# Performance work log

Hardware: AMD Instinct MI355X
Metric: run time of the kernel (lower is better)

## Reference

```python
import jax, jax.numpy as jnp
import numpy as np

B, S, HID, H, DH = 4, 1024, 1024, 16, 64
MAX_REL = 16
SCALE = 1.0 / (DH ** 0.5)


def _rel_bias(emb, seq_len):
    # Shaw-style relative position bias: emb is [2*MAX_REL+1, DH]
    pos = jnp.arange(seq_len)
    dist = jnp.clip(pos[None, :] - pos[:, None], -MAX_REL, MAX_REL) + MAX_REL
    return emb[dist]  # [S, S, DH]


def setup_inputs() -> dict:
    key = jax.random.key(0)
    ks = jax.random.split(key, 14)
    n = jax.random.normal
    w = 0.02
    return {
        "query": n(ks[0], (B, S, HID), dtype=jnp.float32),
        "key": n(ks[1], (B, S, HID), dtype=jnp.float32),
        "value": n(ks[2], (B, S, HID), dtype=jnp.float32),
        # per-head projection weights stacked over heads
        "Wq": n(ks[3], (H, HID, DH), dtype=jnp.float32) * w,
        "bq": n(ks[4], (H, DH), dtype=jnp.float32) * w,
        "Wk": n(ks[5], (H, HID, DH), dtype=jnp.float32) * w,
        "bk": n(ks[6], (H, DH), dtype=jnp.float32) * w,
        "Wv": n(ks[7], (H, HID, DH), dtype=jnp.float32) * w,
        "bv": n(ks[8], (H, DH), dtype=jnp.float32) * w,
        # relative-position embedding tables (shared across heads)
        "rel_k_emb": n(ks[9], (2 * MAX_REL + 1, DH), dtype=jnp.float32) * w,
        "rel_v_emb": n(ks[10], (2 * MAX_REL + 1, DH), dtype=jnp.float32) * w,
        # output projection fc: Linear(hidden, hidden)
        "fc_W": n(ks[11], (HID, HID), dtype=jnp.float32) * w,
        "fc_b": n(ks[12], (HID,), dtype=jnp.float32) * w,
    }


def reference(query, key, value, Wq, bq, Wk, bk, Wv, bv, rel_k_emb, rel_v_emb, fc_W, fc_b):
    # per-head projections, all heads batched: [B, H, S, DH]
    q = jnp.einsum('bsd,hde->bhse', query, Wq) + bq[None, :, None, :]
    k = jnp.einsum('bsd,hde->bhse', key, Wk) + bk[None, :, None, :]
    v = jnp.einsum('bsd,hde->bhse', value, Wv) + bv[None, :, None, :]

    k_bias = _rel_bias(rel_k_emb, S)  # [S, S, DH]
    v_bias = _rel_bias(rel_v_emb, S)  # [S, S, DH]

    # scores: QK^T plus relative-position key bias term
    scores = jnp.einsum('bhqe,bhke->bhqk', q, k)
    scores = scores + jnp.einsum('bhqe,qke->bhqk', q, k_bias)
    attn = jax.nn.softmax(scores * SCALE, axis=-1)  # [B, H, S, S]

    # values: A V plus relative-position value bias term
    out = jnp.einsum('bhqk,bhke->bhqe', attn, v)
    out = out + jnp.einsum('bhqk,qke->bhqe', attn, v_bias)

    # concat heads -> [B, S, HID], then fc
    out = out.transpose(0, 2, 1, 3).reshape(B, S, HID)
    return out @ fc_W.T + fc_b
```

## Files before the change

### kernel.cpp

```cpp
#include <hip/hip_runtime.h>
#include <stdint.h>

#define B_ 4
#define S_ 1024
#define HID_ 1024
#define H_ 16
#define DH_ 64
#define NDIST 33
#define SCALE_ 0.125f

typedef unsigned short u16;
typedef __attribute__((ext_vector_type(8))) short short8;
typedef __attribute__((ext_vector_type(4))) float floatx4;

static __device__ __forceinline__ float bf2f(u16 u) {
  union { unsigned int i; float f; } v; v.i = ((unsigned int)u) << 16; return v.f;
}
static __device__ __forceinline__ u16 f2bf(float x) {
  union { float f; unsigned int i; } v; v.f = x;
  return (u16)((v.i + 0x7FFFu + ((v.i >> 16) & 1u)) >> 16);
}
static __device__ __forceinline__ floatx4 mfma_bf16(short8 a, short8 b, floatx4 c) {
  return __builtin_amdgcn_mfma_f32_16x16x32_bf16(a, b, c, 0, 0, 0);
}
static __device__ __forceinline__ void gload_lds16(const void* g, void* l) {
  __builtin_amdgcn_global_load_lds(
      (const __attribute__((address_space(1))) unsigned int*)g,
      (__attribute__((address_space(3))) unsigned int*)l, 16, 0, 0);
}

#define OFF_BQ   0
#define OFF_BK   1024
#define OFF_BV   2048
#define OFF_RELK 3072
#define OFF_RELV 5184
#define OFF_FCW  7296
#define OFF_FCB  1055872
#define CONV_TOT 1056896

struct SrcPtrs { const void* p[7]; };

__global__ __launch_bounds__(256) void detect_kernel(const u16* __restrict__ q,
                                                     int* __restrict__ flag) {
  __shared__ float red[256];
  float m = 0.f;
  for (int i = threadIdx.x; i < 8192; i += 256) {
    float v = fabsf(bf2f(q[2 * i]));
    m = fmaxf(m, (v < 1e30f) ? v : 1e20f);
  }
  red[threadIdx.x] = m;
  __syncthreads();
  for (int s = 128; s > 0; s >>= 1) {
    if (threadIdx.x < (unsigned)s) red[threadIdx.x] = fmaxf(red[threadIdx.x], red[threadIdx.x + s]);
    __syncthreads();
  }
  if (threadIdx.x == 0) *flag = (red[0] > 1e4f) ? 1 : 0;
}

__global__ __launch_bounds__(256) void convert_kernel(SrcPtrs srcs,
                                                      const int* __restrict__ flag,
                                                      u16* __restrict__ dst) {
  constexpr int segsz[7] = {1024,1024,1024,2112,2112,1048576,1024};
  constexpr int cumE[7]  = {OFF_BQ,OFF_BK,OFF_BV,OFF_RELK,OFF_RELV,OFF_FCW,OFF_FCB};
  constexpr int cumB[8]  = {0,1,2,3,6,9,1033,1034};
  const int bid = blockIdx.x;
  int t = 0;
  #pragma unroll
  for (int i = 1; i < 7; ++i) if (bid >= cumB[i]) t = i;
  const int chunk = (bid - cumB[t]) * 1024 + threadIdx.x * 4;
  if (chunk >= segsz[t]) return;
  __align__(8) u16 o[4];
  if (*flag) {
    const float* s = (const float*)srcs.p[t];
    float4 v = *(const float4*)(s + chunk);
    o[0] = f2bf(v.x); o[1] = f2bf(v.y); o[2] = f2bf(v.z); o[3] = f2bf(v.w);
  } else {
    const u16* s = (const u16*)srcs.p[t];
    *(uint2*)o = *(const uint2*)(s + chunk);
  }
  *(uint2*)(dst + cumE[t] + chunk) = *(const uint2*)o;
}

__global__ __launch_bounds__(256) void qkvconv_kernel(
    const void* __restrict__ qin, const void* __restrict__ kin,
    const void* __restrict__ vin, const int* __restrict__ flag,
    u16* __restrict__ qc, u16* __restrict__ kc, u16* __restrict__ vc)
{
  const int isf = *flag;
  const int total = 3 * (4096 * 1024 / 8);
  for (int g = blockIdx.x * 256 + threadIdx.x; g < total; g += gridDim.x * 256) {
    const int z = g >> 19;
    const int off = (g & 524287) * 8;
    const void* src = (z == 0) ? qin : (z == 1) ? kin : vin;
    u16* dst = (z == 0) ? qc : (z == 1) ? kc : vc;
    if (isf) {
      const float* s = (const float*)src + off;
      float4 v0 = *(const float4*)s;
      float4 v1 = *(const float4*)(s + 4);
      __align__(16) u16 tmp[8] = {f2bf(v0.x),f2bf(v0.y),f2bf(v0.z),f2bf(v0.w),
                                  f2bf(v1.x),f2bf(v1.y),f2bf(v1.z),f2bf(v1.w)};
      *(uint4*)(dst + off) = *(const uint4*)tmp;
    } else {
      *(uint4*)(dst + off) = *(const uint4*)((const u16*)src + off);
    }
  }
}

__global__ __launch_bounds__(256) void wtrans_kernel(
    const void* __restrict__ Wq, const void* __restrict__ Wk, const void* __restrict__ Wv,
    const int* __restrict__ flag, u16* __restrict__ wt)
{
  const int dt = blockIdx.x, h = blockIdx.y, z = blockIdx.z;
  const void* W = (z == 0) ? Wq : (z == 1) ? Wk : Wv;
  const int tid = threadIdx.x;
  const int isf = *flag;
  __shared__ __align__(16) u16 t_l[64 * 72];

  #pragma unroll
  for (int i = 0; i < 2; ++i) {
    int g = tid + 256 * i;
    int d = g & 63, e8 = (g >> 6) * 8;
    size_t off = ((size_t)h * HID_ + dt * 64 + d) * DH_ + e8;
    __align__(16) u16 tmp[8];
    if (isf) {
      const float* Wf = (const float*)W + off;
      float4 v0 = *(const float4*)Wf;
      float4 v1 = *(const float4*)(Wf + 4);
      tmp[0]=f2bf(v0.x); tmp[1]=f2bf(v0.y); tmp[2]=f2bf(v0.z); tmp[3]=f2bf(v0.w);
      tmp[4]=f2bf(v1.x); tmp[5]=f2bf(v1.y); tmp[6]=f2bf(v1.z); tmp[7]=f2bf(v1.w);
    } else {
      *(uint4*)tmp = *(const uint4*)((const u16*)W + off);
    }
    #pragma unroll
    for (int j = 0; j < 8; ++j) {
      int e = e8 + j;
      t_l[e * 72 + (((d >> 3) ^ (e & 7)) << 3) + (d & 7)] = tmp[j];
    }
  }
  __syncthreads();
  {
    int e = tid >> 2, c0 = (tid & 3) * 2;
    u16* dst = wt + ((size_t)(z * H_ + h) * DH_ + e) * HID_ + dt * 64;
    uint4 x0 = *(const uint4*)(t_l + e * 72 + (((c0    ) ^ (e & 7)) << 3));
    uint4 x1 = *(const uint4*)(t_l + e * 72 + (((c0 + 1) ^ (e & 7)) << 3));
    *(uint4*)(dst + c0 * 8)     = x0;
    *(uint4*)(dst + c0 * 8 + 8) = x1;
  }
}

__global__ __launch_bounds__(256, 3) void proj_kernel(
    const u16* __restrict__ qc, const u16* __restrict__ kc, const u16* __restrict__ vc,
    const u16* __restrict__ wt, const u16* __restrict__ conv,
    u16* __restrict__ qo, u16* __restrict__ ko, u16* __restrict__ vo)
{
  const int bid = blockIdx.x + 32 * (blockIdx.y + 8 * blockIdx.z);
  const int xcd = bid & 7, local = bid >> 3;
  const int p  = xcd * 3 + (local >> 5);
  const int rt = local & 31;
  const int z  = p >> 3, ct = p & 7;

  const u16* A    = (z == 0) ? qc : (z == 1) ? kc : vc;
  const u16* Wz   = wt + (size_t)z * (H_ * DH_ * HID_);
  const u16* bias = conv + ((z == 0) ? OFF_BQ : (z == 1) ? OFF_BK : OFF_BV);
  u16*       O    = (z == 0) ? qo : (z == 1) ? ko : vo;
  const int tid = threadIdx.x, lane = tid & 63, w = tid >> 6, quad = lane >> 4, l16 = lane & 15;

  __shared__ __align__(16) u16 a_l[2][128 * 32];
  __shared__ __align__(16) u16 b_l[2][128 * 32];

  floatx4 acc[4][4];
  #pragma unroll
  for (int i = 0; i < 4; ++i)
    #pragma unroll
    for (int j = 0; j < 4; ++j) acc[i][j] = (floatx4){0.f,0.f,0.f,0.f};

  const int mq = (w & 1) * 64, nq = (w >> 1) * 64;
  const int u = (lane & 3) ^ ((lane >> 3) & 3);
  const int cs = (quad ^ ((l16 >> 1) & 3)) * 8;

  auto STAGE = [&](int bu, int kk) {
    #pragma unroll
    for (int i = 0; i < 2; ++i) {
      int row = (tid + 256 * i) >> 2;
      gload_lds16(A  + (size_t)(rt * 128 + row) * HID_ + kk * 32 + u * 8,
                  a_l[bu] + (w * 64 + i * 256) * 8);
      gload_lds16(Wz + (size_t)(ct * 128 + row) * HID_ + kk * 32 + u * 8,
                  b_l[bu] + (w * 64 + i * 256) * 8);
    }
  };

  STAGE(0, 0);
  int cur = 0;
  for (int kk = 0; kk < 32; ++kk) {
    __syncthreads();
    if (kk + 1 < 32) STAGE(cur ^ 1, kk + 1);
    const u16* ab = a_l[cur];
    const u16* bb = b_l[cur];
    short8 af[4], bfr[4];
    #pragma unroll
    for (int i = 0; i < 4; ++i) {
      af[i]  = *(const short8*)(ab + (mq + i * 16 + l16) * 32 + cs);
      bfr[i] = *(const short8*)(bb + (nq + i * 16 + l16) * 32 + cs);
    }
    #pragma unroll
    for (int i = 0; i < 4; ++i)
      #pragma unroll
      for (int j = 0; j < 4; ++j)
        acc[i][j] = mfma_bf16(af[i], bfr[j], acc[i][j]);
    cur ^= 1;
  }

  #pragma unroll
  for (int j = 0; j < 4; ++j) {
    int col = ct * 128 + nq + j * 16 + l16;
    int hh = col >> 6, e = col & 63;
    float bb = bf2f(bias[hh * 64 + e]);
    #pragma unroll
    for (int i = 0; i < 4; ++i) {
      #pragma unroll
      for (int r = 0; r < 4; ++r) {
        int m = rt * 128 + mq + i * 16 + quad * 4 + r;
        int bidx = m >> 10, srow = m & 1023;
        O[(((size_t)(bidx * H_ + hh)) * S_ + srow) * DH_ + e] = f2bf(acc[i][j][r] + bb);
      }
    }
  }
}

__global__ __launch_bounds__(256, 4) void attn_kernel(
    const u16* __restrict__ Q, const u16* __restrict__ K, const u16* __restrict__ V,
    const u16* __restrict__ conv, u16* __restrict__ Ox)
{
  const int bid = blockIdx.x + 16 * (blockIdx.y + 16 * blockIdx.z);
  const int nid = (bid & 7) * 128 + (bid >> 3);
  const int qt = nid & 15, h = (nid >> 4) & 15, b = nid >> 8;

  const int tid = threadIdx.x;
  const int lane = tid & 63, w = tid >> 6, quad = lane >> 4, l16 = lane & 15;
  const size_t base = ((size_t)(b * H_ + h)) * S_ * DH_;
  const u16* Kb = K + base;
  const u16* Vb = V + base;

  __shared__ __align__(16) char smem[40320];
  u16*   p_l    = (u16*)(smem);
  u16*   q_l    = p_l;
  u16*   k_l    = (u16*)(smem + 9216);
  u16*   vt_l   = (u16*)(smem + 18432);
  u16*   rq_l   = (u16*)(smem + 27648);
  float* bucket = (float*)(smem + 31872);
  u16*   rkb    = (u16*)(smem + 31872);

  uint4 kr0 = *(const uint4*)(Kb + (size_t)(tid >> 3) * DH_ + (tid & 7) * 8);
  uint4 kr1 = *(const uint4*)(Kb + (size_t)((tid >> 3) + 32) * DH_ + (tid & 7) * 8);
  uint4 vr0 = *(const uint4*)(Vb + (size_t)lane * DH_ + w * 16);
  uint4 vr1 = *(const uint4*)(Vb + (size_t)lane * DH_ + w * 16 + 8);

  #pragma unroll
  for (int i = 0; i < 2; ++i) {
    int idx = tid + 256 * i;
    int row = idx >> 3, c8 = (idx & 7) * 8;
    *(uint4*)(q_l + row * 72 + c8) =
        *(const uint4*)(Q + base + (size_t)(qt * 64 + row) * DH_ + c8);
  }
  const u16* relk = conv + OFF_RELK;
  for (int idx = tid; idx < 48 * 8; idx += 256) {
    int row = idx >> 3, c8 = (idx & 7) * 8;
    uint4 v = make_uint4(0, 0, 0, 0);
    if (row < NDIST) v = *(const uint4*)(relk + row * 64 + c8);
    *(uint4*)(rkb + row * 72 + c8) = v;
  }
  __syncthreads();

  const int m0 = w * 16;
  short8 qa0 = *(const short8*)(q_l + (m0 + l16) * 72 + quad * 8);
  short8 qa1 = *(const short8*)(q_l + (m0 + l16) * 72 + 32 + quad * 8);

  floatx4 c_d0 = {0.f,0.f,0.f,0.f}, c_d32 = {0.f,0.f,0.f,0.f};
  #pragma unroll
  for (int t3 = 0; t3 < 3; ++t3) {
    floatx4 c = {0.f,0.f,0.f,0.f};
    c = mfma_bf16(qa0, *(const short8*)(rkb + (t3 * 16 + l16) * 72 + quad * 8), c);
    c = mfma_bf16(qa1, *(const short8*)(rkb + (t3 * 16 + l16) * 72 + 32 + quad * 8), c);
    if (t3 == 0) c_d0 = c;
    if (t3 == 2) c_d32 = c;
    int d = t3 * 16 + l16;
    if (d < NDIST) {
      #pragma unroll
      for (int r = 0; r < 4; ++r) rq_l[(m0 + quad * 4 + r) * 33 + d] = f2bf(c[r]);
    }
  }
  float rqs_lo[4], rqs_hi[4];
  #pragma unroll
  for (int r = 0; r < 4; ++r) {
    rqs_lo[r] = bf2f(f2bf(__shfl(c_d0[r],  lane & 48, 64))) * SCALE_;
    rqs_hi[r] = bf2f(f2bf(__shfl(c_d32[r], lane & 48, 64))) * SCALE_;
  }
  __syncthreads();
  for (int idx = tid; idx < 64 * 33; idx += 256) bucket[idx] = 0.f;

  floatx4 o[4], oi = {0.f,0.f,0.f,0.f};
  #pragma unroll
  for (int t = 0; t < 4; ++t) o[t] = (floatx4){0.f,0.f,0.f,0.f};

  for (int kt = 0; kt < 16; ++kt) {
    __syncthreads();
    *(uint4*)(k_l + (tid >> 3) * 72 + (tid & 7) * 8) = kr0;
    *(uint4*)(k_l + ((tid >> 3) + 32) * 72 + (tid & 7) * 8) = kr1;
    {
      const u16* t8 = (const u16*)&vr0;
      #pragma unroll
      for (int j = 0; j < 8; ++j) vt_l[(w * 16 + j) * 72 + lane] = t8[j];
      const u16* t9 = (const u16*)&vr1;
      #pragma unroll
      for (int j = 0; j < 8; ++j) vt_l[(w * 16 + 8 + j) * 72 + lane] = t9[j];
    }
    __syncthreads();
    if (kt < 15) {
      const size_t kb = (size_t)((kt + 1) * 64);
      kr0 = *(const uint4*)(Kb + (kb + (tid >> 3)) * DH_ + (tid & 7) * 8);
      kr1 = *(const uint4*)(Kb + (kb + (tid >> 3) + 32) * DH_ + (tid & 7) * 8);
      vr0 = *(const uint4*)(Vb + (kb + lane) * DH_ + w * 16);
      vr1 = *(const uint4*)(Vb + (kb + lane) * DH_ + w * 16 + 8);
    }

    const int dkt = kt - qt;
    const bool near = (dkt >= -1) && (dkt <= 1);

    #pragma unroll
    for (int t = 0; t < 4; ++t) {
      floatx4 s = {0.f,0.f,0.f,0.f};
      s = mfma_bf16(qa0, *(const short8*)(k_l + (t * 16 + l16) * 72 + quad * 8), s);
      s = mfma_bf16(qa1, *(const short8*)(k_l + (t * 16 + l16) * 72 + 32 + quad * 8), s);
      int kcol = t * 16 + l16;
      if (near) {
        #pragma unroll
        for (int r = 0; r < 4; ++r) {
          int m = m0 + quad * 4 + r;
          int delta = (kt * 64 + kcol) - (qt * 64 + m);
          int dist = (delta < -16 ? -16 : (delta > 16 ? 16 : delta)) + 16;
          float logit = (s[r] + bf2f(rq_l[m * 33 + dist])) * SCALE_;
          u16 pu = f2bf(__expf(fminf(logit, 30.f)));
          p_l[m * 72 + kcol] = pu;
          float pv = bf2f(pu);
          float vhi = (dist == 32) ? pv : 0.f;
          float vlo = (dist == 0) ? pv : 0.f;
          #pragma unroll
          for (int off2 = 1; off2 < 16; off2 <<= 1) {
            vhi += __shfl_xor(vhi, off2, 16);
            vlo += __shfl_xor(vlo, off2, 16);
          }
          if (l16 == 0) {
            if (vhi != 0.f) atomicAdd(&bucket[m * 33 + 32], vhi);
            if (vlo != 0.f) atomicAdd(&bucket[m * 33 + 0], vlo);
          }
          if (dist > 0 && dist < 32) atomicAdd(&bucket[m * 33 + dist], pv);
        }
      } else {
        #pragma unroll
        for (int r = 0; r < 4; ++r) {
          int m = m0 + quad * 4 + r;
          float logit = fmaf(s[r], SCALE_, (dkt < 0) ? rqs_lo[r] : rqs_hi[r]);
          u16 pu = f2bf(__expf(fminf(logit, 30.f)));
          p_l[m * 72 + kcol] = pu;
        }
      }
    }

    u16 iv = ((l16 == 0 && dkt <= -2) || (l16 == 1 && dkt >= 2)) ? (u16)0x3F80 : (u16)0;
    short8 ib;
    #pragma unroll
    for (int j = 0; j < 8; ++j) ib[j] = (short)iv;
    short8 pa0 = *(const short8*)(p_l + (m0 + l16) * 72 + quad * 8);
    short8 pa1 = *(const short8*)(p_l + (m0 + l16) * 72 + 32 + quad * 8);
    oi = mfma_bf16(pa0, ib, oi);
    oi = mfma_bf16(pa1, ib, oi);
    #pragma unroll
    for (int t = 0; t < 4; ++t) {
      int e = t * 16 + l16;
      short8 vb0 = *(const short8*)(vt_l + e * 72 + quad * 8);
      short8 vb1 = *(const short8*)(vt_l + e * 72 + 32 + quad * 8);
      o[t] = mfma_bf16(pa0, vb0, o[t]);
      o[t] = mfma_bf16(pa1, vb1, o[t]);
    }
  }

  __syncthreads();
  if (l16 == 0) {
    #pragma unroll
    for (int r = 0; r < 4; ++r) bucket[(m0 + quad * 4 + r) * 33 + 0] += oi[r];
  } else if (l16 == 1) {
    #pragma unroll
    for (int r = 0; r < 4; ++r) bucket[(m0 + quad * 4 + r) * 33 + 32] += oi[r];
  }
  __syncthreads();

  u16* rvT = k_l;
  u16* Bf  = p_l;
  for (int idx = tid; idx < 576; idx += 256) {
    ((uint4*)rvT)[idx] = make_uint4(0, 0, 0, 0);
    ((uint4*)Bf)[idx]  = make_uint4(0, 0, 0, 0);
  }
  __syncthreads();
  const u16* relv = conv + OFF_RELV;
  for (int idx = tid; idx < NDIST * 64; idx += 256) {
    int d = idx >> 6, e = idx & 63;
    rvT[e * 72 + d] = relv[idx];
  }
  for (int idx = tid; idx < 64 * NDIST; idx += 256) {
    int m = idx / NDIST, d = idx - m * NDIST;
    Bf[m * 72 + d] = f2bf(bucket[m * 33 + d]);
  }
  __syncthreads();

  short8 ba0 = *(const short8*)(Bf + (m0 + l16) * 72 + quad * 8);
  short8 ba1 = *(const short8*)(Bf + (m0 + l16) * 72 + 32 + quad * 8);
  #pragma unroll
  for (int t = 0; t < 4; ++t) {
    short8 rb0 = *(const short8*)(rvT + (t * 16 + l16) * 72 + quad * 8);
    short8 rb1 = *(const short8*)(rvT + (t * 16 + l16) * 72 + 32 + quad * 8);
    o[t] = mfma_bf16(ba0, rb0, o[t]);
    o[t] = mfma_bf16(ba1, rb1, o[t]);
  }

  float rl[4];
  #pragma unroll
  for (int r = 0; r < 4; ++r) {
    int m = m0 + quad * 4 + r;
    float s = 0.f;
    #pragma unroll
    for (int d = 0; d < NDIST; ++d) s += bucket[m * 33 + d];
    rl[r] = 1.f / s;
  }

  #pragma unroll
  for (int t = 0; t < 4; ++t) {
    int e = t * 16 + l16;
    #pragma unroll
    for (int r = 0; r < 4; ++r) {
      int srow = qt * 64 + m0 + quad * 4 + r;
      Ox[((size_t)(b * S_ + srow)) * HID_ + h * 64 + e] = f2bf(o[t][r] * rl[r]);
    }
  }
}

__global__ __launch_bounds__(256, 3) void fc_kernel(
    const u16* __restrict__ X, const u16* __restrict__ conv,
    const int* __restrict__ flag, void* __restrict__ outv)
{
  const u16* Wf  = conv + OFF_FCW;
  const u16* bfc = conv + OFF_FCB;
  const int bid = blockIdx.x + 32 * blockIdx.y;
  const int ct = bid & 7, rt = bid >> 3;
  const int tid = threadIdx.x, lane = tid & 63, w = tid >> 6, quad = lane >> 4, l16 = lane & 15;
  const int isf = *flag;

  __shared__ __align__(16) u16 a_l[2][128 * 32];
  __shared__ __align__(16) u16 b_l[2][128 * 32];

  floatx4 acc[4][4];
  #pragma unroll
  for (int i = 0; i < 4; ++i)
    #pragma unroll
    for (int j = 0; j < 4; ++j) acc[i][j] = (floatx4){0.f,0.f,0.f,0.f};

  const int mq = (w & 1) * 64, nq = (w >> 1) * 64;
  const int u = (lane & 3) ^ ((lane >> 3) & 3);
  const int cs = (quad ^ ((l16 >> 1) & 3)) * 8;

  auto STAGE = [&](int bu, int kk) {
    #pragma unroll
    for (int i = 0; i < 2; ++i) {
      int row = (tid + 256 * i) >> 2;
      gload_lds16(X  + (size_t)(rt * 128 + row) * HID_ + kk * 32 + u * 8,
                  a_l[bu] + (w * 64 + i * 256) * 8);
      gload_lds16(Wf + (size_t)(ct * 128 + row) * HID_ + kk * 32 + u * 8,
                  b_l[bu] + (w * 64 + i * 256) * 8);
    }
  };

  STAGE(0, 0);
  int cur = 0;
  for (int kk = 0; kk < 32; ++kk) {
    __syncthreads();
    if (kk + 1 < 32) STAGE(cur ^ 1, kk + 1);
    const u16* ab = a_l[cur];
    const u16* bb = b_l[cur];
    short8 af[4], bfr[4];
    #pragma unroll
    for (int i = 0; i < 4; ++i) {
      af[i]  = *(const short8*)(ab + (mq + i * 16 + l16) * 32 + cs);
      bfr[i] = *(const short8*)(bb + (nq + i * 16 + l16) * 32 + cs);
    }
    #pragma unroll
    for (int i = 0; i < 4; ++i)
      #pragma unroll
      for (int j = 0; j < 4; ++j)
        acc[i][j] = mfma_bf16(af[i], bfr[j], acc[i][j]);
    cur ^= 1;
  }

  #pragma unroll
  for (int j = 0; j < 4; ++j) {
    int col = ct * 128 + nq + j * 16 + l16;
    float bb = bf2f(bfc[col]);
    #pragma unroll
    for (int i = 0; i < 4; ++i) {
      #pragma unroll
      for (int r = 0; r < 4; ++r) {
        int m = rt * 128 + mq + i * 16 + quad * 4 + r;
        float val = acc[i][j][r] + bb;
        size_t idx = (size_t)m * HID_ + col;
        if (isf) ((float*)outv)[idx] = val;
        else     ((u16*)outv)[idx]   = f2bf(val);
      }
    }
  }
}

extern "C" void kernel_launch(void* const* d_in, const int* in_sizes, int n_in,
                              void* d_out, int out_size, void* d_ws, size_t ws_size,
                              hipStream_t stream) {
  int* flag = (int*)d_ws;
  u16* conv = (u16*)((char*)d_ws + 16);
  u16* wt   = conv + CONV_TOT;
  u16* qw   = wt + 3145728;
  u16* kw   = qw + 4194304;
  u16* vw   = kw + 4194304;
  u16* xw   = vw + 4194304;
  u16* qc   = xw;
  u16* kc   = xw + 4194304;
  u16* vc   = kc + 4194304;

  detect_kernel<<<1, 256, 0, stream>>>((const u16*)d_in[0], flag);

  SrcPtrs sp;
  sp.p[0] = d_in[4];  sp.p[1] = d_in[6];  sp.p[2] = d_in[8];
  sp.p[3] = d_in[9];  sp.p[4] = d_in[10]; sp.p[5] = d_in[11]; sp.p[6] = d_in[12];
  convert_kernel<<<1034, 256, 0, stream>>>(sp, flag, conv);
  qkvconv_kernel<<<2048, 256, 0, stream>>>(d_in[0], d_in[1], d_in[2], flag, qc, kc, vc);

  wtrans_kernel<<<dim3(16, 16, 3), 256, 0, stream>>>(d_in[3], d_in[5], d_in[7], flag, wt);
  proj_kernel<<<dim3(32, 8, 3), 256, 0, stream>>>(qc, kc, vc, wt, conv, qw, kw, vw);
  attn_kernel<<<dim3(16, 16, 4), 256, 0, stream>>>(qw, kw, vw, conv, xw);
  fc_kernel<<<dim3(32, 8), 256, 0, stream>>>(xw, conv, flag, (u16*)d_out);
}
```

Baseline: 295.8 us.

## Transpose QK^T MFMA operands so each lane owns a query row

```diff
diff --git a/kernel.cpp b/kernel.cpp
--- a/kernel.cpp
+++ b/kernel.cpp
@@ -252,8 +252,9 @@
 
   uint4 kr0 = *(const uint4*)(Kb + (size_t)(tid >> 3) * DH_ + (tid & 7) * 8);
   uint4 kr1 = *(const uint4*)(Kb + (size_t)((tid >> 3) + 32) * DH_ + (tid & 7) * 8);
-  uint4 vr0 = *(const uint4*)(Vb + (size_t)lane * DH_ + w * 16);
-  uint4 vr1 = *(const uint4*)(Vb + (size_t)lane * DH_ + w * 16 + 8);
+  __align__(16) u16 vtmp[16];
+  #pragma unroll
+  for (int j = 0; j < 16; ++j) vtmp[j] = Vb[(size_t)(w * 16 + j) * DH_ + lane];
 
   #pragma unroll
   for (int i = 0; i < 2; ++i) {
@@ -272,6 +273,7 @@
   __syncthreads();
 
   const int m0 = w * 16;
+  const int mrow = m0 + l16;
   short8 qa0 = *(const short8*)(q_l + (m0 + l16) * 72 + quad * 8);
   short8 qa1 = *(const short8*)(q_l + (m0 + l16) * 72 + 32 + quad * 8);
 
@@ -289,11 +291,17 @@
       for (int r = 0; r < 4; ++r) rq_l[(m0 + quad * 4 + r) * 33 + d] = f2bf(c[r]);
     }
   }
-  float rqs_lo[4], rqs_hi[4];
-  #pragma unroll
-  for (int r = 0; r < 4; ++r) {
-    rqs_lo[r] = bf2f(f2bf(__shfl(c_d0[r],  lane & 48, 64))) * SCALE_;
-    rqs_hi[r] = bf2f(f2bf(__shfl(c_d32[r], lane & 48, 64))) * SCALE_;
+  float rqs_lo, rqs_hi;
+  {
+    float t0 = 0.f, t2 = 0.f;
+    #pragma unroll
+    for (int r = 0; r < 4; ++r) {
+      float a  = __shfl(c_d0[r],  (l16 >> 2) * 16, 64);
+      float bb = __shfl(c_d32[r], (l16 >> 2) * 16, 64);
+      if ((l16 & 3) == r) { t0 = a; t2 = bb; }
+    }
+    rqs_lo = bf2f(f2bf(t0)) * SCALE_;
+    rqs_hi = bf2f(f2bf(t2)) * SCALE_;
   }
   __syncthreads();
   for (int idx = tid; idx < 64 * 33; idx += 256) bucket[idx] = 0.f;
@@ -306,63 +314,58 @@
     __syncthreads();
     *(uint4*)(k_l + (tid >> 3) * 72 + (tid & 7) * 8) = kr0;
     *(uint4*)(k_l + ((tid >> 3) + 32) * 72 + (tid & 7) * 8) = kr1;
-    {
-      const u16* t8 = (const u16*)&vr0;
-      #pragma unroll
-      for (int j = 0; j < 8; ++j) vt_l[(w * 16 + j) * 72 + lane] = t8[j];
-      const u16* t9 = (const u16*)&vr1;
-      #pragma unroll
-      for (int j = 0; j < 8; ++j) vt_l[(w * 16 + 8 + j) * 72 + lane] = t9[j];
-    }
+    *(uint4*)(vt_l + lane * 72 + w * 16)     = *(const uint4*)(vtmp);
+    *(uint4*)(vt_l + lane * 72 + w * 16 + 8) = *(const uint4*)(vtmp + 8);
     __syncthreads();
     if (kt < 15) {
       const size_t kb = (size_t)((kt + 1) * 64);
       kr0 = *(const uint4*)(Kb + (kb + (tid >> 3)) * DH_ + (tid & 7) * 8);
       kr1 = *(const uint4*)(Kb + (kb + (tid >> 3) + 32) * DH_ + (tid & 7) * 8);
-      vr0 = *(const uint4*)(Vb + (kb + lane) * DH_ + w * 16);
-      vr1 = *(const uint4*)(Vb + (kb + lane) * DH_ + w * 16 + 8);
+      #pragma unroll
+      for (int j = 0; j < 16; ++j) vtmp[j] = Vb[(kb + w * 16 + j) * DH_ + lane];
     }
 
     const int dkt = kt - qt;
     const bool near = (dkt >= -1) && (dkt <= 1);
+    float vlo = 0.f, vhi = 0.f;
 
     #pragma unroll
     for (int t = 0; t < 4; ++t) {
       floatx4 s = {0.f,0.f,0.f,0.f};
-      s = mfma_bf16(qa0, *(const short8*)(k_l + (t * 16 + l16) * 72 + quad * 8), s);
-      s = mfma_bf16(qa1, *(const short8*)(k_l + (t * 16 + l16) * 72 + 32 + quad * 8), s);
-      int kcol = t * 16 + l16;
+      short8 ka0 = *(const short8*)(k_l + (t * 16 + l16) * 72 + quad * 8);
+      short8 ka1 = *(const short8*)(k_l + (t * 16 + l16) * 72 + 32 + quad * 8);
+      s = mfma_bf16(ka0, qa0, s);
+      s = mfma_bf16(ka1, qa1, s);
+      __align__(8) u16 pk[4];
       if (near) {
         #pragma unroll
         for (int r = 0; r < 4; ++r) {
-          int m = m0 + quad * 4 + r;
-          int delta = (kt * 64 + kcol) - (qt * 64 + m);
+          int delta = dkt * 64 + t * 16 + quad * 4 + r - mrow;
           int dist = (delta < -16 ? -16 : (delta > 16 ? 16 : delta)) + 16;
-          float logit = (s[r] + bf2f(rq_l[m * 33 + dist])) * SCALE_;
+          float logit = (s[r] + bf2f(rq_l[mrow * 33 + dist])) * SCALE_;
           u16 pu = f2bf(__expf(fminf(logit, 30.f)));
-          p_l[m * 72 + kcol] = pu;
+          pk[r] = pu;
           float pv = bf2f(pu);
-          float vhi = (dist == 32) ? pv : 0.f;
-          float vlo = (dist == 0) ? pv : 0.f;
-          #pragma unroll
-          for (int off2 = 1; off2 < 16; off2 <<= 1) {
-            vhi += __shfl_xor(vhi, off2, 16);
-            vlo += __shfl_xor(vlo, off2, 16);
-          }
-          if (l16 == 0) {
-            if (vhi != 0.f) atomicAdd(&bucket[m * 33 + 32], vhi);
-            if (vlo != 0.f) atomicAdd(&bucket[m * 33 + 0], vlo);
-          }
-          if (dist > 0 && dist < 32) atomicAdd(&bucket[m * 33 + dist], pv);
+          if (dist == 0)       vlo += pv;
+          else if (dist == 32) vhi += pv;
+          else                 bucket[mrow * 33 + dist] = pv;
         }
       } else {
+        float rqs = (dkt < 0) ? rqs_lo : rqs_hi;
         #pragma unroll
         for (int r = 0; r < 4; ++r) {
-          int m = m0 + quad * 4 + r;
-          float logit = fmaf(s[r], SCALE_, (dkt < 0) ? rqs_lo[r] : rqs_hi[r]);
-          u16 pu = f2bf(__expf(fminf(logit, 30.f)));
-          p_l[m * 72 + kcol] = pu;
+          float logit = fmaf(s[r], SCALE_, rqs);
+          pk[r] = f2bf(__expf(fminf(logit, 30.f)));
         }
+      }
+      *(uint2*)(p_l + mrow * 72 + t * 16 + quad * 4) = *(const uint2*)pk;
+    }
+    if (near) {
+      vlo += __shfl_xor(vlo, 16); vlo += __shfl_xor(vlo, 32);
+      vhi += __shfl_xor(vhi, 16); vhi += __shfl_xor(vhi, 32);
+      if (quad == 0) {
+        if (vlo != 0.f) atomicAdd(&bucket[mrow * 33 + 0], vlo);
+        if (vhi != 0.f) atomicAdd(&bucket[mrow * 33 + 32], vhi);
       }
     }
 
```

Measured after the change: 266.0 us. 1.11x faster.
